# Kernel tuning notes

Hardware: AMD Instinct MI355X
Metric: run time of the kernel (lower is better)

The kernel has to match this reference:

```python
import jax, jax.numpy as jnp
import numpy as np

N, E, IN, HID, OUT = 50000, 800000, 128, 64, 32
ALPHA, BETA, DIVIDER = 0.5, 0.5, 5.0


def _gcn_conv(x, edge_index, W, b, alpha=ALPHA, beta=BETA):
    """DirectedGCNConv.forward: add self loops, linear, degree-normalized gather-mul-scatter."""
    n = x.shape[0]
    loops = jnp.arange(n, dtype=edge_index.dtype)
    row = jnp.concatenate([edge_index[0], loops])  # sources
    col = jnp.concatenate([edge_index[1], loops])  # targets
    x = x @ W.T + b                                # [n, out]
    ones = jnp.ones(row.shape[0], dtype=x.dtype)
    in_deg = jax.ops.segment_sum(ones, col, num_segments=n)
    out_deg = jax.ops.segment_sum(ones, row, num_segments=n)
    norm = in_deg[col] ** (-alpha) * out_deg[row] ** (-beta)  # [E+n]
    msgs = norm[:, None] * x[row]                  # gather + scale
    return jax.ops.segment_sum(msgs, col, num_segments=n)  # scatter-add aggr


def _source_enc(x, ei, W1, b1, W2, b2):
    x = jax.nn.relu(_gcn_conv(x, ei, W1, b1))
    return _gcn_conv(x, jnp.flip(ei, axis=0), W2, b2)


def _target_enc(x, ei, W1, b1, W2, b2):
    x = jax.nn.relu(_gcn_conv(x, jnp.flip(ei, axis=0), W1, b1))
    return _gcn_conv(x, ei, W2, b2)


def setup_inputs() -> dict:
    key = jax.random.key(0)
    ks = jax.random.split(key, 24)

    def lin(kw, kb, o, i, scale):
        return (jax.random.normal(kw, (o, i), jnp.float32) * scale,
                jax.random.normal(kb, (o,), jnp.float32) * 0.01)

    s1 = (2.0 / (IN + HID)) ** 0.5
    s2 = (2.0 / (HID + OUT)) ** 0.5
    inp = {
        "s": jax.random.normal(ks[0], (N, IN), jnp.float32),
        "t": jax.random.normal(ks[1], (N, IN), jnp.float32),
        "edge_index": jax.random.randint(ks[2], (2, E), 0, N, jnp.int32),
        "noise_s": jax.random.normal(ks[3], (N, OUT), jnp.float32),
        "noise_t": jax.random.normal(ks[4], (N, OUT), jnp.float32),
    }
    names = ["sm", "sl", "tm", "tl"]  # source/target mu/logstd encoders
    k = 5
    for nm in names:
        W1, b1 = lin(ks[k], ks[k + 1], HID, IN, s1); k += 2
        W2, b2 = lin(ks[k], ks[k + 1], OUT, HID, s2); k += 2
        inp[nm + "1_W"], inp[nm + "1_b"] = W1, b1
        inp[nm + "2_W"], inp[nm + "2_b"] = W2, b2
    return inp


def reference(s, t, edge_index, noise_s, noise_t,
              sm1_W, sm1_b, sm2_W, sm2_b,
              sl1_W, sl1_b, sl2_W, sl2_b,
              tm1_W, tm1_b, tm2_W, tm2_b,
              tl1_W, tl1_b, tl2_W, tl2_b):
    s_mu = _source_enc(s, edge_index, sm1_W, sm1_b, sm2_W, sm2_b)
    s_logstd = _source_enc(s, edge_index, sl1_W, sl1_b, sl2_W, sl2_b)
    t_mu = _target_enc(t, edge_index, tm1_W, tm1_b, tm2_W, tm2_b)
    t_logstd = _target_enc(t, edge_index, tl1_W, tl1_b, tl2_W, tl2_b)
    # reparametrize_edges (training mode), noise materialized as input
    s_out = s_mu + noise_s * jnp.exp(s_logstd) / DIVIDER
    t_out = t_mu + noise_t * jnp.exp(t_logstd) / DIVIDER
    return (s_out, t_out)
```

## Files before the change

### kernel.cpp

```cpp
#include <hip/hip_runtime.h>
#include <hip/hip_fp16.h>
#include <math.h>

#define N_NODES 50000
#define NPACK 25000
#define E_EDGES 800000
#define NCHUNKS ((N_NODES + 1023) / 1024)
#define LIN_BLOCKS 1564
#define QCH 64
#define CHUNK (E_EDGES / QCH)
#define CHUNK4 (CHUNK / 4)
#define OCT_NODES 6250
#define OCT_PACK 3125
#define HF_BLOCKS 1024
#define HL_GRID (HF_BLOCKS + LIN_BLOCKS)
#define LCAP 2048

typedef _Float16 half8 __attribute__((ext_vector_type(8)));
typedef float f32x4 __attribute__((ext_vector_type(4)));

__device__ inline float fac_from(unsigned int u) {
    unsigned short us = (unsigned short)(u >> 16);
    __half h;
    __builtin_memcpy(&h, &us, 2);
    return __half2float(h);
}

__device__ inline int unpack_cnt(const unsigned int* cntp, int i) {
    unsigned int w = cntp[i >> 1];
    return (i & 1) ? (int)(w >> 16) : (int)(w & 0xffff);
}

__global__ __launch_bounds__(256) void w2h_kernel(const float* __restrict__ sW2a,
                                                  const float* __restrict__ sW2b,
                                                  const float* __restrict__ tW2a,
                                                  const float* __restrict__ tW2b,
                                                  __half* __restrict__ hw2) {
    int i = blockIdx.x * 256 + threadIdx.x;
    if (i >= 4 * 2048) return;
    const float* src[4] = { sW2a, sW2b, tW2a, tW2b };
    hw2[i] = __float2half(src[i >> 11][i & 2047]);
}

__global__ __launch_bounds__(256) void hist_lin1_kernel(const int* __restrict__ ei0,
                                                        const int* __restrict__ ei1,
                                                        unsigned int* __restrict__ ghist,
                                                        unsigned short* __restrict__ list,
                                                        unsigned int* __restrict__ cnt_bkt,
                                                        const float* __restrict__ Xs,
                                                        const float* __restrict__ Xt,
                                                        const float* __restrict__ sWa,
                                                        const float* __restrict__ sba,
                                                        const float* __restrict__ sWb,
                                                        const float* __restrict__ sbb,
                                                        const float* __restrict__ tWa,
                                                        const float* __restrict__ tba,
                                                        const float* __restrict__ tWb,
                                                        const float* __restrict__ tbb,
                                                        __half* __restrict__ As,
                                                        __half* __restrict__ At, int n) {
    __shared__ unsigned int h[OCT_PACK];
    __shared__ unsigned int lcnt;
    int bx = blockIdx.x;
    int tid = threadIdx.x;
    if (bx < HF_BLOCKS) {
        int oct = bx & 7, q = (bx >> 3) & 63, dir = bx >> 9;
        for (int i = tid; i < OCT_PACK; i += 256) h[i] = 0;
        if (tid == 0) lcnt = 0;
        __syncthreads();
        const int* key = dir ? ei0 : ei1;
        const uint4* key4 = (const uint4*)(key + q * CHUNK);
        unsigned short* lst = list + ((size_t)(dir * QCH + q) * 8 + oct) * LCAP;
        int lo = oct * OCT_NODES;
        int lane = tid & 63;
        for (int j = tid; j < CHUNK4; j += 256) {
            uint4 k4 = key4[j];
            int vv[4] = { (int)k4.x, (int)k4.y, (int)k4.z, (int)k4.w };
#pragma unroll
            for (int e = 0; e < 4; ++e) {
                unsigned int d = (unsigned int)(vv[e] - lo);
                bool pred = d < OCT_NODES;
                if (pred) atomicAdd(&h[d >> 1], 1u << ((d & 1) * 16));
                unsigned long long m = __ballot(pred);
                if (m) {
                    int pre = __popcll(m & ((1ull << lane) - 1));
                    int tot = __popcll(m);
                    int ldr = __ffsll((unsigned long long)m) - 1;
                    unsigned int base = 0;
                    if (lane == ldr) base = atomicAdd(&lcnt, (unsigned int)tot);
                    base = __shfl(base, ldr);
                    unsigned int slot = base + (unsigned int)pre;
                    if (pred && slot < LCAP) lst[slot] = (unsigned short)(j * 4 + e);
                }
            }
        }
        __syncthreads();
        unsigned int* g = ghist + (size_t)(dir * QCH + q) * NPACK + oct * OCT_PACK;
        for (int i = tid; i < OCT_PACK; i += 256) g[i] = h[i];
        if (tid == 0) cnt_bkt[dir * 512 + q * 8 + oct] = (lcnt < LCAP) ? lcnt : LCAP;
        return;
    }
    int lidx = bx - HF_BLOCKS;
    int y = lidx & 1;
    int xb = lidx >> 1;
    const float* X = y ? Xt : Xs;
    const float* Wset[2] = { y ? tWa : sWa, y ? tWb : sWb };
    const float* bset[2] = { y ? tba : sba, y ? tbb : sbb };
    __half* A = y ? At : As;

    int w = tid >> 6, lane = tid & 63;
    int quad = lane >> 4, col = lane & 15;
    int node0 = xb * 64 + w * 16;

    half8 afrag[4];
    {
        int row = node0 + col;
        if (row >= n) row = n - 1;
        const float* xr = X + (size_t)row * 128 + quad * 8;
#pragma unroll
        for (int kc = 0; kc < 4; ++kc) {
            float4 f0 = *(const float4*)(xr + kc * 32);
            float4 f1 = *(const float4*)(xr + kc * 32 + 4);
            half8 hh;
            hh[0] = (_Float16)f0.x; hh[1] = (_Float16)f0.y;
            hh[2] = (_Float16)f0.z; hh[3] = (_Float16)f0.w;
            hh[4] = (_Float16)f1.x; hh[5] = (_Float16)f1.y;
            hh[6] = (_Float16)f1.z; hh[7] = (_Float16)f1.w;
            afrag[kc] = hh;
        }
    }

#pragma unroll
    for (int set = 0; set < 2; ++set) {
        const float* Ws = Wset[set];
#pragma unroll
        for (int nt = 0; nt < 4; ++nt) {
            float bb = bset[set][nt * 16 + col];
            f32x4 acc = { bb, bb, bb, bb };
            const float* wr = Ws + (size_t)(nt * 16 + col) * 128 + quad * 8;
#pragma unroll
            for (int kc = 0; kc < 4; ++kc) {
                float4 f0 = *(const float4*)(wr + kc * 32);
                float4 f1 = *(const float4*)(wr + kc * 32 + 4);
                half8 bfr;
                bfr[0] = (_Float16)f0.x; bfr[1] = (_Float16)f0.y;
                bfr[2] = (_Float16)f0.z; bfr[3] = (_Float16)f0.w;
                bfr[4] = (_Float16)f1.x; bfr[5] = (_Float16)f1.y;
                bfr[6] = (_Float16)f1.z; bfr[7] = (_Float16)f1.w;
                acc = __builtin_amdgcn_mfma_f32_16x16x32_f16(afrag[kc], bfr, acc, 0, 0, 0);
            }
#pragma unroll
            for (int r = 0; r < 4; ++r) {
                int node = node0 + quad * 4 + r;
                if (node < n)
                    A[(size_t)node * 128 + set * 64 + nt * 16 + col] = __float2half(acc[r]);
            }
        }
    }
}

__global__ __launch_bounds__(256) void nodescan_kernel(unsigned int* __restrict__ ghist,
                                                       unsigned int* __restrict__ cntp) {
    int vp = blockIdx.x * 256 + threadIdx.x;
    int dir = blockIdx.y;
    if (vp >= NPACK) return;
    unsigned int lo = 0, hi = 0;
    unsigned int* g = ghist + (size_t)dir * QCH * NPACK + vp;
#pragma unroll 4
    for (int q = 0; q < QCH; ++q) {
        unsigned int w = g[(size_t)q * NPACK];
        g[(size_t)q * NPACK] = lo | (hi << 16);
        lo += w & 0xffff;
        hi += w >> 16;
    }
    cntp[dir * NPACK + vp] = lo | (hi << 16);
}

__global__ __launch_bounds__(1024) void scan_chunk2_kernel(const unsigned int* __restrict__ cntp,
                                                           int* __restrict__ offs_f,
                                                           int* __restrict__ offs_b,
                                                           int* __restrict__ part_f,
                                                           int* __restrict__ part_b, int n) {
    const unsigned int* cnt = cntp + (blockIdx.y ? NPACK : 0);
    int* offs = blockIdx.y ? offs_b : offs_f;
    int* partials = blockIdx.y ? part_b : part_f;
    __shared__ int sh[1024];
    int tid = threadIdx.x;
    int i = blockIdx.x * 1024 + tid;
    int v = (i < n) ? unpack_cnt(cnt, i) : 0;
    sh[tid] = v;
    __syncthreads();
    for (int off = 1; off < 1024; off <<= 1) {
        int add = (tid >= off) ? sh[tid - off] : 0;
        __syncthreads();
        sh[tid] += add;
        __syncthreads();
    }
    if (i < n) offs[i] = sh[tid] - v;
    if (tid == 1023) partials[blockIdx.x] = sh[tid];
}

__global__ __launch_bounds__(64) void scan_partials2_kernel(int* part_f, int* part_b, int nchunks) {
    int* p = blockIdx.x ? part_b : part_f;
    __shared__ int sh[64];
    int tid = threadIdx.x;
    int v = (tid < nchunks) ? p[tid] : 0;
    sh[tid] = v;
    __syncthreads();
    for (int off = 1; off < 64; off <<= 1) {
        int add = (tid >= off) ? sh[tid - off] : 0;
        __syncthreads();
        sh[tid] += add;
        __syncthreads();
    }
    if (tid < nchunks) p[tid] = sh[tid] - v;
    if (tid == 63) p[nchunks] = sh[63];
}

__global__ __launch_bounds__(256) void addback_deg_kernel(int* __restrict__ offs_f,
                                                          int* __restrict__ offs_b,
                                                          const int* __restrict__ part_f,
                                                          const int* __restrict__ part_b,
                                                          const unsigned int* __restrict__ cntp,
                                                          float* dsi, float* dti,
                                                          unsigned short* __restrict__ h_dsi,
                                                          unsigned short* __restrict__ h_dti,
                                                          int n, int nchunks) {
    int i = blockIdx.x * 256 + threadIdx.x;
    if (blockIdx.y == 0) {
        if (i < n) {
            offs_f[i] += part_f[i >> 10];
            float f = rsqrtf((float)(unpack_cnt(cntp, i) + 1));
            dti[i] = f;
            __half hf = __float2half(f);
            unsigned short hb; __builtin_memcpy(&hb, &hf, 2);
            h_dti[i] = hb;
        } else if (i == n) offs_f[n] = part_f[nchunks];
    } else {
        if (i < n) {
            offs_b[i] += part_b[i >> 10];
            float f = rsqrtf((float)(unpack_cnt(cntp + NPACK, i) + 1));
            dsi[i] = f;
            __half hf = __float2half(f);
            unsigned short hb; __builtin_memcpy(&hb, &hf, 2);
            h_dsi[i] = hb;
        } else if (i == n) offs_b[n] = part_b[nchunks];
    }
}

__global__ __launch_bounds__(256) void fill_kernel(const int* __restrict__ ei0,
                                                   const int* __restrict__ ei1,
                                                   const unsigned int* __restrict__ ghist,
                                                   const int* __restrict__ offs_f,
                                                   const int* __restrict__ offs_b,
                                                   const unsigned short* __restrict__ h_dsi,
                                                   const unsigned short* __restrict__ h_dti,
                                                   unsigned int* __restrict__ pay_f,
                                                   unsigned int* __restrict__ pay_b,
                                                   const unsigned short* __restrict__ list,
                                                   const unsigned int* __restrict__ cnt_bkt) {
    __shared__ unsigned int pos[OCT_NODES];
    int bx = blockIdx.x;
    int oct = bx & 7, q = (bx >> 3) & 63, dir = bx >> 9;
    int tid = threadIdx.x;
    const unsigned int* pref = ghist + (size_t)(dir * QCH + q) * NPACK + oct * OCT_PACK;
    const int* offs = dir ? offs_b : offs_f;
    int lo = oct * OCT_NODES;
    for (int d = tid; d < OCT_NODES; d += 256) {
        unsigned int pw = pref[d >> 1];
        int cb = (d & 1) ? (int)(pw >> 16) : (int)(pw & 0xffff);
        pos[d] = (unsigned int)(offs[lo + d] + cb);
    }
    __syncthreads();
    const int* key = dir ? ei0 : ei1;
    const int* pid = dir ? ei1 : ei0;
    const unsigned short* hfac = dir ? h_dti : h_dsi;
    unsigned int* pay = dir ? pay_b : pay_f;
    const unsigned short* lst = list + ((size_t)(dir * QCH + q) * 8 + oct) * LCAP;
    int cnt = (int)cnt_bkt[dir * 512 + q * 8 + oct];
    int base = q * CHUNK;
    for (int j = tid; j < cnt; j += 256) {
        int gi = base + (int)lst[j];
        int v = key[gi];
        int id = pid[gi];
        unsigned int p = atomicAdd(&pos[v - lo], 1u);
        unsigned int hb = hfac[id];
        pay[p] = (unsigned int)id | (hb << 16);
    }
}

__device__ inline void acc_fma(float* acc, uint4 u, float f) {
    const __half2* h = (const __half2*)&u;
    float2 f0 = __half22float2(h[0]);
    float2 f1 = __half22float2(h[1]);
    float2 f2 = __half22float2(h[2]);
    float2 f3 = __half22float2(h[3]);
    acc[0] += f * f0.x; acc[1] += f * f0.y; acc[2] += f * f1.x; acc[3] += f * f1.y;
    acc[4] += f * f2.x; acc[5] += f * f2.y; acc[6] += f * f3.x; acc[7] += f * f3.y;
}

__global__ __launch_bounds__(256) void pull_lin2_kernel(const __half* __restrict__ As,
                                                        const __half* __restrict__ At,
                                                        __half* __restrict__ Cs,
                                                        __half* __restrict__ Ct,
                                                        const int* __restrict__ offs_f,
                                                        const int* __restrict__ offs_b,
                                                        const unsigned int* __restrict__ pay_f,
                                                        const unsigned int* __restrict__ pay_b,
                                                        const float* __restrict__ dsi,
                                                        const float* __restrict__ dti,
                                                        const float* __restrict__ sb2a,
                                                        const float* __restrict__ sb2b,
                                                        const float* __restrict__ tb2a,
                                                        const float* __restrict__ tb2b,
                                                        const __half* __restrict__ hw2, int n) {
    int y = blockIdx.y;
    const __half* xw = y ? At : As;
    __half* C = y ? Ct : Cs;
    const int* offs = y ? offs_b : offs_f;
    const unsigned int* pay = y ? pay_b : pay_f;
    const float* fac_self  = y ? dsi : dti;
    const float* fac_other = y ? dti : dsi;
    const float* b2a = y ? tb2a : sb2a;
    const float* b2b = y ? tb2b : sb2b;

    __shared__ __half xsh[16 * 136];

    int tid = threadIdx.x;
    int ln = tid >> 4;
    int f4 = tid & 15;
    int v = blockIdx.x * 16 + ln;
    int i = offs[v], end = offs[v + 1];
    const uint4* xw16 = (const uint4*)xw;

    float acc[8] = {0, 0, 0, 0, 0, 0, 0, 0};
    acc_fma(acc, xw16[v * 16 + f4], fac_other[v]);
    while (i < end && (i & 3)) {
        unsigned int pk = pay[i];
        acc_fma(acc, xw16[(pk & 0xffff) * 16 + f4], fac_from(pk));
        ++i;
    }
    for (; i + 3 < end; i += 4) {
        uint4 pk = *(const uint4*)(pay + i);
        int s0 = pk.x & 0xffff, s1 = pk.y & 0xffff;
        int s2 = pk.z & 0xffff, s3 = pk.w & 0xffff;
        uint4 ua = xw16[s0 * 16 + f4];
        uint4 ub = xw16[s1 * 16 + f4];
        uint4 uc = xw16[s2 * 16 + f4];
        uint4 ud = xw16[s3 * 16 + f4];
        acc_fma(acc, ua, fac_from(pk.x));
        acc_fma(acc, ub, fac_from(pk.y));
        acc_fma(acc, uc, fac_from(pk.z));
        acc_fma(acc, ud, fac_from(pk.w));
    }
    for (; i < end; ++i) {
        unsigned int pk = pay[i];
        acc_fma(acc, xw16[(pk & 0xffff) * 16 + f4], fac_from(pk));
    }

    float fs = fac_self[v];
    half8 hx;
#pragma unroll
    for (int j = 0; j < 8; ++j) hx[j] = (_Float16)fmaxf(acc[j] * fs, 0.0f);
    *(half8*)&xsh[ln * 136 + f4 * 8] = hx;
    __syncthreads();

    int w = tid >> 6, lane = tid & 63;
    int s = w >> 1, nt = w & 1;
    int quad = lane >> 4, col = lane & 15;
    float bb = (s ? b2b : b2a)[nt * 16 + col];
    f32x4 cacc = { bb, bb, bb, bb };
    const __half* hw = hw2 + (size_t)(y * 2 + s) * 2048;
#pragma unroll
    for (int t = 0; t < 2; ++t) {
        half8 af = *(const half8*)&xsh[col * 136 + s * 64 + t * 32 + quad * 8];
        half8 bf = *(const half8*)&hw[(nt * 16 + col) * 64 + t * 32 + quad * 8];
        cacc = __builtin_amdgcn_mfma_f32_16x16x32_f16(af, bf, cacc, 0, 0, 0);
    }
    int vbase = blockIdx.x * 16 + quad * 4;
    int o = s * 32 + nt * 16 + col;
#pragma unroll
    for (int r = 0; r < 4; ++r)
        C[(size_t)(vbase + r) * 64 + o] = __float2half(cacc[r]);
}

__global__ __launch_bounds__(256) void final_pull2_kernel(const __half* __restrict__ Cs,
                                                          const __half* __restrict__ Ct,
                                                          float* __restrict__ out_s,
                                                          float* __restrict__ out_t,
                                                          const int* __restrict__ offs_f,
                                                          const int* __restrict__ offs_b,
                                                          const unsigned int* __restrict__ pay_f,
                                                          const unsigned int* __restrict__ pay_b,
                                                          const float* __restrict__ dsi,
                                                          const float* __restrict__ dti,
                                                          const float* __restrict__ noise_s,
                                                          const float* __restrict__ noise_t,
                                                          int n) {
    int y = blockIdx.y;
    const __half* xw = y ? Ct : Cs;
    float* out = y ? out_t : out_s;
    const int* offs = y ? offs_f : offs_b;
    const unsigned int* pay = y ? pay_f : pay_b;
    const float* fac_self  = y ? dti : dsi;
    const float* fac_other = y ? dsi : dti;
    const float* noise = y ? noise_t : noise_s;

    const uint4* xw16 = (const uint4*)xw;
    int ln = threadIdx.x >> 3;
    int f4 = threadIdx.x & 7;
    int v = blockIdx.x * 32 + ln;
    if (v >= n) return;
    int i = offs[v], end = offs[v + 1];

    float acc[8] = {0, 0, 0, 0, 0, 0, 0, 0};
    acc_fma(acc, xw16[v * 8 + f4], fac_other[v]);
    while (i < end && (i & 3)) {
        unsigned int pk = pay[i];
        acc_fma(acc, xw16[(pk & 0xffff) * 8 + f4], fac_from(pk));
        ++i;
    }
    for (; i + 3 < end; i += 4) {
        uint4 pk = *(const uint4*)(pay + i);
        int s0 = pk.x & 0xffff, s1 = pk.y & 0xffff;
        int s2 = pk.z & 0xffff, s3 = pk.w & 0xffff;
        uint4 ua = xw16[s0 * 8 + f4];
        uint4 ub = xw16[s1 * 8 + f4];
        uint4 uc = xw16[s2 * 8 + f4];
        uint4 ud = xw16[s3 * 8 + f4];
        acc_fma(acc, ua, fac_from(pk.x));
        acc_fma(acc, ub, fac_from(pk.y));
        acc_fma(acc, uc, fac_from(pk.z));
        acc_fma(acc, ud, fac_from(pk.w));
    }
    for (; i < end; ++i) {
        unsigned int pk = pay[i];
        acc_fma(acc, xw16[(pk & 0xffff) * 8 + f4], fac_from(pk));
    }

    float fs = fac_self[v];
#pragma unroll
    for (int j = 0; j < 8; ++j) acc[j] *= fs;

    int lane = threadIdx.x & 63;
    float lg[8];
#pragma unroll
    for (int j = 0; j < 8; ++j) lg[j] = __shfl(acc[j], lane + 4);
    if (f4 < 4) {
        const float4* nz4 = (const float4*)noise;
        float4 n0 = nz4[v * 8 + f4 * 2];
        float4 n1 = nz4[v * 8 + f4 * 2 + 1];
        float4 r0, r1;
        r0.x = acc[0] + n0.x * expf(lg[0]) * 0.2f;
        r0.y = acc[1] + n0.y * expf(lg[1]) * 0.2f;
        r0.z = acc[2] + n0.z * expf(lg[2]) * 0.2f;
        r0.w = acc[3] + n0.w * expf(lg[3]) * 0.2f;
        r1.x = acc[4] + n1.x * expf(lg[4]) * 0.2f;
        r1.y = acc[5] + n1.y * expf(lg[5]) * 0.2f;
        r1.z = acc[6] + n1.z * expf(lg[6]) * 0.2f;
        r1.w = acc[7] + n1.w * expf(lg[7]) * 0.2f;
        float4* o4 = (float4*)out;
        o4[v * 8 + f4 * 2]     = r0;
        o4[v * 8 + f4 * 2 + 1] = r1;
    }
}

extern "C" void kernel_launch(void* const* d_in, const int* in_sizes, int n_in,
                              void* d_out, int out_size, void* d_ws, size_t ws_size,
                              hipStream_t stream) {
    const float* s       = (const float*)d_in[0];
    const float* t       = (const float*)d_in[1];
    const int*   ei      = (const int*)d_in[2];
    const float* noise_s = (const float*)d_in[3];
    const float* noise_t = (const float*)d_in[4];
    const float* sm1_W = (const float*)d_in[5];  const float* sm1_b = (const float*)d_in[6];
    const float* sm2_W = (const float*)d_in[7];  const float* sm2_b = (const float*)d_in[8];
    const float* sl1_W = (const float*)d_in[9];  const float* sl1_b = (const float*)d_in[10];
    const float* sl2_W = (const float*)d_in[11]; const float* sl2_b = (const float*)d_in[12];
    const float* tm1_W = (const float*)d_in[13]; const float* tm1_b = (const float*)d_in[14];
    const float* tm2_W = (const float*)d_in[15]; const float* tm2_b = (const float*)d_in[16];
    const float* tl1_W = (const float*)d_in[17]; const float* tl1_b = (const float*)d_in[18];
    const float* tl2_W = (const float*)d_in[19]; const float* tl2_b = (const float*)d_in[20];

    const int* ei0 = ei;
    const int* ei1 = ei + E_EDGES;

    __half* A_s = (__half*)d_ws;
    __half* A_t = A_s + (size_t)N_NODES * 128;
    __half* C_s = A_t + (size_t)N_NODES * 128;
    __half* C_t = C_s + (size_t)N_NODES * 64;
    unsigned int* pay_fwd = (unsigned int*)(C_t + (size_t)N_NODES * 64);
    unsigned int* pay_bwd = pay_fwd + E_EDGES;
    float* dsi = (float*)(pay_bwd + E_EDGES);
    float* dti = dsi + N_NODES;
    int* offs_fwd = (int*)(dti + N_NODES);
    int* offs_bwd = offs_fwd + N_NODES + 1;
    unsigned int* cntp = (unsigned int*)(offs_bwd + N_NODES + 1);
    int* part_fwd = (int*)(cntp + 2 * NPACK);
    int* part_bwd = part_fwd + NCHUNKS + 1;
    unsigned short* h_dsi = (unsigned short*)(part_bwd + NCHUNKS + 1);
    unsigned short* h_dti = h_dsi + N_NODES;
    unsigned short* list  = h_dti + N_NODES;
    unsigned int* cnt_bkt = (unsigned int*)(list + (size_t)HF_BLOCKS * LCAP);
    __half* hw2 = (__half*)(((uintptr_t)(cnt_bkt + 1024) + 15) & ~(uintptr_t)15);

    unsigned int* ghist = (unsigned int*)C_s;

    float* s_out = (float*)d_out;
    float* t_out = (float*)d_out + N_NODES * 32;

    dim3 blk(256);
    dim3 agrid((N_NODES + 1 + 255) / 256, 2);
    dim3 pgrid(N_NODES / 16, 2);
    dim3 fgrid((N_NODES + 31) / 32, 2);
    dim3 nsgrid((NPACK + 255) / 256, 2);

    w2h_kernel<<<32, blk, 0, stream>>>(sm2_W, sl2_W, tm2_W, tl2_W, hw2);
    hist_lin1_kernel<<<HL_GRID, blk, 0, stream>>>(
        ei0, ei1, ghist, list, cnt_bkt,
        s, t, sm1_W, sm1_b, sl1_W, sl1_b, tm1_W, tm1_b, tl1_W, tl1_b,
        A_s, A_t, N_NODES);
    nodescan_kernel<<<nsgrid, blk, 0, stream>>>(ghist, cntp);
    scan_chunk2_kernel<<<dim3(NCHUNKS, 2), 1024, 0, stream>>>(
        cntp, offs_fwd, offs_bwd, part_fwd, part_bwd, N_NODES);
    scan_partials2_kernel<<<2, 64, 0, stream>>>(part_fwd, part_bwd, NCHUNKS);
    addback_deg_kernel<<<agrid, blk, 0, stream>>>(offs_fwd, offs_bwd, part_fwd, part_bwd,
                                                  cntp, dsi, dti, h_dsi, h_dti,
                                                  N_NODES, NCHUNKS);
    fill_kernel<<<HF_BLOCKS, blk, 0, stream>>>(ei0, ei1, ghist, offs_fwd, offs_bwd,
                                               h_dsi, h_dti, pay_fwd, pay_bwd,
                                               list, cnt_bkt);

    pull_lin2_kernel<<<pgrid, blk, 0, stream>>>(A_s, A_t, C_s, C_t,
                                                offs_fwd, offs_bwd, pay_fwd, pay_bwd,
                                                dsi, dti,
                                                sm2_b, sl2_b, tm2_b, tl2_b, hw2, N_NODES);
    final_pull2_kernel<<<fgrid, blk, 0, stream>>>(C_s, C_t, s_out, t_out,
                                                  offs_fwd, offs_bwd, pay_fwd, pay_bwd,
                                                  dsi, dti, noise_s, noise_t, N_NODES);
}
```

Measured before the change: 321.5 us.

## Halve histogram blocks with quarter-range buckets; fill blocks filter shared lists

The histogram phase now splits the node range into quarters instead of eighths. It uses 512 blocks with a 12500-node shared-memory histogram and a larger per-bucket edge list, so each edge-key chunk is scanned four times instead of eight. The fill kernel keeps 1024 blocks over eighth ranges; each pair of fill blocks reads the same quarter list and drops entries outside its own half. The wave-aggregated ballot/popcount slot reservation is replaced by a plain per-lane shared atomic on the list counter. This cuts redundant key scanning but adds shared-atomic contention and doubles the list reads in fill.

```diff
diff --git a/kernel.cpp b/kernel.cpp
--- a/kernel.cpp
+++ b/kernel.cpp
@@ -10,11 +10,14 @@
 #define QCH 64
 #define CHUNK (E_EDGES / QCH)
 #define CHUNK4 (CHUNK / 4)
-#define OCT_NODES 6250
-#define OCT_PACK 3125
-#define HF_BLOCKS 1024
-#define HL_GRID (HF_BLOCKS + LIN_BLOCKS)
-#define LCAP 2048
+#define OCT_NODES 12500
+#define OCT_PACK 6250
+#define HIST_BLOCKS 512
+#define HL_GRID (HIST_BLOCKS + LIN_BLOCKS)
+#define FOCT_NODES 6250
+#define FOCT_PACK 3125
+#define FILL_BLOCKS 1024
+#define LCAP 4096
 
 typedef _Float16 half8 __attribute__((ext_vector_type(8)));
 typedef float f32x4 __attribute__((ext_vector_type(4)));
@@ -63,44 +66,35 @@
     __shared__ unsigned int lcnt;
     int bx = blockIdx.x;
     int tid = threadIdx.x;
-    if (bx < HF_BLOCKS) {
-        int oct = bx & 7, q = (bx >> 3) & 63, dir = bx >> 9;
+    if (bx < HIST_BLOCKS) {
+        int oct = bx & 3, q = (bx >> 2) & 63, dir = bx >> 8;
         for (int i = tid; i < OCT_PACK; i += 256) h[i] = 0;
         if (tid == 0) lcnt = 0;
         __syncthreads();
         const int* key = dir ? ei0 : ei1;
         const uint4* key4 = (const uint4*)(key + q * CHUNK);
-        unsigned short* lst = list + ((size_t)(dir * QCH + q) * 8 + oct) * LCAP;
+        unsigned short* lst = list + ((size_t)(dir * QCH + q) * 4 + oct) * LCAP;
         int lo = oct * OCT_NODES;
-        int lane = tid & 63;
         for (int j = tid; j < CHUNK4; j += 256) {
             uint4 k4 = key4[j];
             int vv[4] = { (int)k4.x, (int)k4.y, (int)k4.z, (int)k4.w };
 #pragma unroll
             for (int e = 0; e < 4; ++e) {
                 unsigned int d = (unsigned int)(vv[e] - lo);
-                bool pred = d < OCT_NODES;
-                if (pred) atomicAdd(&h[d >> 1], 1u << ((d & 1) * 16));
-                unsigned long long m = __ballot(pred);
-                if (m) {
-                    int pre = __popcll(m & ((1ull << lane) - 1));
-                    int tot = __popcll(m);
-                    int ldr = __ffsll((unsigned long long)m) - 1;
-                    unsigned int base = 0;
-                    if (lane == ldr) base = atomicAdd(&lcnt, (unsigned int)tot);
-                    base = __shfl(base, ldr);
-                    unsigned int slot = base + (unsigned int)pre;
-                    if (pred && slot < LCAP) lst[slot] = (unsigned short)(j * 4 + e);
+                if (d < OCT_NODES) {
+                    atomicAdd(&h[d >> 1], 1u << ((d & 1) * 16));
+                    unsigned int slot = atomicAdd(&lcnt, 1u);
+                    if (slot < LCAP) lst[slot] = (unsigned short)(j * 4 + e);
                 }
             }
         }
         __syncthreads();
         unsigned int* g = ghist + (size_t)(dir * QCH + q) * NPACK + oct * OCT_PACK;
         for (int i = tid; i < OCT_PACK; i += 256) g[i] = h[i];
-        if (tid == 0) cnt_bkt[dir * 512 + q * 8 + oct] = (lcnt < LCAP) ? lcnt : LCAP;
+        if (tid == 0) cnt_bkt[dir * 256 + q * 4 + oct] = (lcnt < LCAP) ? lcnt : LCAP;
         return;
     }
-    int lidx = bx - HF_BLOCKS;
+    int lidx = bx - HIST_BLOCKS;
     int y = lidx & 1;
     int xb = lidx >> 1;
     const float* X = y ? Xt : Xs;
@@ -259,14 +253,15 @@
                                                    unsigned int* __restrict__ pay_b,
                                                    const unsigned short* __restrict__ list,
                                                    const unsigned int* __restrict__ cnt_bkt) {
-    __shared__ unsigned int pos[OCT_NODES];
+    __shared__ unsigned int pos[FOCT_NODES];
     int bx = blockIdx.x;
-    int oct = bx & 7, q = (bx >> 3) & 63, dir = bx >> 9;
+    int foct = bx & 7, q = (bx >> 3) & 63, dir = bx >> 9;
+    int oct = foct >> 1;
     int tid = threadIdx.x;
-    const unsigned int* pref = ghist + (size_t)(dir * QCH + q) * NPACK + oct * OCT_PACK;
+    const unsigned int* pref = ghist + (size_t)(dir * QCH + q) * NPACK + foct * FOCT_PACK;
     const int* offs = dir ? offs_b : offs_f;
-    int lo = oct * OCT_NODES;
-    for (int d = tid; d < OCT_NODES; d += 256) {
+    int lo = foct * FOCT_NODES;
+    for (int d = tid; d < FOCT_NODES; d += 256) {
         unsigned int pw = pref[d >> 1];
         int cb = (d & 1) ? (int)(pw >> 16) : (int)(pw & 0xffff);
         pos[d] = (unsigned int)(offs[lo + d] + cb);
@@ -276,16 +271,19 @@
     const int* pid = dir ? ei1 : ei0;
     const unsigned short* hfac = dir ? h_dti : h_dsi;
     unsigned int* pay = dir ? pay_b : pay_f;
-    const unsigned short* lst = list + ((size_t)(dir * QCH + q) * 8 + oct) * LCAP;
-    int cnt = (int)cnt_bkt[dir * 512 + q * 8 + oct];
+    const unsigned short* lst = list + ((size_t)(dir * QCH + q) * 4 + oct) * LCAP;
+    int cnt = (int)cnt_bkt[dir * 256 + q * 4 + oct];
     int base = q * CHUNK;
     for (int j = tid; j < cnt; j += 256) {
         int gi = base + (int)lst[j];
         int v = key[gi];
-        int id = pid[gi];
-        unsigned int p = atomicAdd(&pos[v - lo], 1u);
-        unsigned int hb = hfac[id];
-        pay[p] = (unsigned int)id | (hb << 16);
+        unsigned int d = (unsigned int)(v - lo);
+        if (d < FOCT_NODES) {
+            int id = pid[gi];
+            unsigned int p = atomicAdd(&pos[d], 1u);
+            unsigned int hb = hfac[id];
+            pay[p] = (unsigned int)id | (hb << 16);
+        }
     }
 }
 
@@ -501,8 +499,8 @@
     unsigned short* h_dsi = (unsigned short*)(part_bwd + NCHUNKS + 1);
     unsigned short* h_dti = h_dsi + N_NODES;
     unsigned short* list  = h_dti + N_NODES;
-    unsigned int* cnt_bkt = (unsigned int*)(list + (size_t)HF_BLOCKS * LCAP);
-    __half* hw2 = (__half*)(((uintptr_t)(cnt_bkt + 1024) + 15) & ~(uintptr_t)15);
+    unsigned int* cnt_bkt = (unsigned int*)(list + (size_t)HIST_BLOCKS * LCAP);
+    __half* hw2 = (__half*)(((uintptr_t)(cnt_bkt + 512) + 15) & ~(uintptr_t)15);
 
     unsigned int* ghist = (unsigned int*)C_s;
 
@@ -527,9 +525,9 @@
     addback_deg_kernel<<<agrid, blk, 0, stream>>>(offs_fwd, offs_bwd, part_fwd, part_bwd,
                                                   cntp, dsi, dti, h_dsi, h_dti,
                                                   N_NODES, NCHUNKS);
-    fill_kernel<<<HF_BLOCKS, blk, 0, stream>>>(ei0, ei1, ghist, offs_fwd, offs_bwd,
-                                               h_dsi, h_dti, pay_fwd, pay_bwd,
-                                               list, cnt_bkt);
+    fill_kernel<<<FILL_BLOCKS, blk, 0, stream>>>(ei0, ei1, ghist, offs_fwd, offs_bwd,
+                                                 h_dsi, h_dti, pay_fwd, pay_bwd,
+                                                 list, cnt_bkt);
 
     pull_lin2_kernel<<<pgrid, blk, 0, stream>>>(A_s, A_t, C_s, C_t,
                                                 offs_fwd, offs_bwd, pay_fwd, pay_bwd,
```

Result: no change. 323.6 us (+0.6%).
